# Kernel optimization log

Measured on AMD Instinct MI355X. Metric: run time of the kernel, lower is better.

Reference implementation:

```python
import jax, jax.numpy as jnp
import numpy as np

N = 100000
E = 1600000
ENC_EDGE = 32
ENC_NODE = 64
HIDDEN = 128


def setup_inputs() -> dict:
    key = jax.random.key(0)
    ks = jax.random.split(key, 8)
    x = jax.random.normal(ks[0], (N, ENC_NODE), dtype=jnp.float32)
    edge_index = jax.random.randint(ks[1], (2, E), 0, N, dtype=jnp.int64)
    edge_attr = jax.random.normal(ks[2], (E, ENC_EDGE), dtype=jnp.float32)
    u = jax.random.normal(ks[3], (256, ENC_NODE), dtype=jnp.float32)
    batch = jax.random.randint(ks[4], (N,), 0, 256, dtype=jnp.int64)
    # mlp1: Lin(ENC_EDGE+ENC_NODE -> HIDDEN), xavier_uniform weight, bias=0.01
    in1 = ENC_EDGE + ENC_NODE
    lim1 = float(np.sqrt(6.0 / (in1 + HIDDEN)))
    W1 = jax.random.uniform(ks[5], (in1, HIDDEN), minval=-lim1, maxval=lim1, dtype=jnp.float32)
    b1 = jnp.full((HIDDEN,), 0.01, dtype=jnp.float32)
    # mlp2: Lin(HIDDEN+ENC_NODE -> ENC_NODE)
    in2 = HIDDEN + ENC_NODE
    lim2 = float(np.sqrt(6.0 / (in2 + ENC_NODE)))
    W2 = jax.random.uniform(ks[6], (in2, ENC_NODE), minval=-lim2, maxval=lim2, dtype=jnp.float32)
    b2 = jnp.full((ENC_NODE,), 0.01, dtype=jnp.float32)
    return {"x": x, "edge_index": edge_index, "edge_attr": edge_attr,
            "u": u, "batch": batch, "W1": W1, "b1": b1, "W2": W2, "b2": b2}


def reference(x, edge_index, edge_attr, u, batch, W1, b1, W2, b2):
    row, col = edge_index[0], edge_index[1]
    # gather source node features, concat edge features -> [E, 96]
    msg = jnp.concatenate([x[row], edge_attr], axis=1)
    # mlp1 -> [E, HIDDEN]
    msg = msg @ W1 + b1
    # scatter_add into destination nodes -> [N, HIDDEN]
    agg = jax.ops.segment_sum(msg, col, num_segments=x.shape[0])
    # concat with node features, mlp2 -> [N, ENC_NODE]
    out = jnp.concatenate([x, agg], axis=1)
    return out @ W2 + b2
```

## Files before the change

### kernel.cpp

```cpp
#include <hip/hip_runtime.h>

#define NN 100000
#define NE 1600000
#define CAP 32
#define OVF_CAP 65536


__device__ __forceinline__ float mcat_val(const float* __restrict__ W1,
                                          const float* __restrict__ W2,
                                          int r, int j) {
    if (r < 64) return W2[r * 64 + j];
    float acc = 0.f;
    if (r < 128) {
        int i = r - 64;
        for (int h = 0; h < 128; ++h)
            acc = fmaf(W1[i * 128 + h], W2[(64 + h) * 64 + j], acc);
    } else {
        int i = r - 128;
        for (int h = 0; h < 128; ++h)
            acc = fmaf(W1[(64 + i) * 128 + h], W2[(64 + h) * 64 + j], acc);
    }
    return acc;
}

__global__ void precompute_kernel(const float* __restrict__ W1,
                                  const float* __restrict__ b1,
                                  const float* __restrict__ W2,
                                  float* __restrict__ Mcat,
                                  float* __restrict__ vb) {
    int idx = blockIdx.x * blockDim.x + threadIdx.x;
    if (idx < 160 * 64) {
        int kb = idx >> 8, j = (idx >> 2) & 63, w = idx & 3;
        Mcat[idx] = mcat_val(W1, W2, kb * 4 + w, j);
    } else if (idx < 160 * 64 + 64) {
        int j = idx - 160 * 64;
        float acc = 0.f;
        for (int h = 0; h < 128; ++h)
            acc = fmaf(b1[h], W2[(64 + h) * 64 + j], acc);
        vb[j] = acc;
    }
}

__global__ void fill_kernel(const int* __restrict__ ei,
                            int* __restrict__ cnt,
                            int* __restrict__ ovf_cnt,
                            int2* __restrict__ slots,
                            int4* __restrict__ ovf) {
    int i = blockIdx.x * blockDim.x + threadIdx.x;
    int stride = gridDim.x * blockDim.x;
    for (int e = i; e < NE; e += stride) {
        int src = ei[e];
        int dst = ei[NE + e];
        int pos = atomicAdd(&cnt[dst], 1);
        if (pos < CAP) {
            slots[dst * CAP + pos] = make_int2(src, e);
        } else {
            int op = atomicAdd(ovf_cnt, 1);
            if (op < OVF_CAP) ovf[op] = make_int4(dst, src, e, 0);
        }
    }
}

__global__ __launch_bounds__(1024, 2)
void gather_kernel(const float* __restrict__ x,
                   const float* __restrict__ ea,
                   const float* __restrict__ b2,
                   const float* __restrict__ Mcat,
                   const float* __restrict__ vb,
                   const int* __restrict__ cnt,
                   const int2* __restrict__ slots,
                   float* __restrict__ out) {
    __shared__ __align__(16) float m4[40 * 256];
    __shared__ __align__(16) float v_lds[16][160];
    __shared__ int p_lds[16][64];
    __shared__ float vb_lds[64], b2_lds[64];

    for (int i = threadIdx.x; i < 10240; i += 1024) m4[i] = Mcat[i];
    if (threadIdx.x < 64) {
        vb_lds[threadIdx.x] = vb[threadIdx.x];
        b2_lds[threadIdx.x] = b2[threadIdx.x];
    }
    __syncthreads();

    int wave = threadIdx.x >> 6;
    int lane = threadIdx.x & 63;
    int elane = lane & 31;
    int nwt = gridDim.x * 16;

    for (int n = blockIdx.x * 16 + wave; n < NN; n += nwt) {
        int dcnt = cnt[n];
        int m = dcnt < CAP ? dcnt : CAP;
        p_lds[wave][lane] = ((const int*)slots)[(size_t)n * 64 + lane];
        __threadfence_block();
        const int2* pr = (const int2*)p_lds[wave];

        float xa0 = 0.f, xa1 = 0.f, xa2 = 0.f, xa3 = 0.f;
        float e0a = 0.f, e1a = 0.f;
        int i = 0;
        for (; i + 4 <= m; i += 4) {
            int2 q0 = pr[i], q1 = pr[i + 1], q2 = pr[i + 2], q3 = pr[i + 3];
            xa0 += x[(size_t)q0.x * 64 + lane];
            xa1 += x[(size_t)q1.x * 64 + lane];
            xa2 += x[(size_t)q2.x * 64 + lane];
            xa3 += x[(size_t)q3.x * 64 + lane];
            int eA = (lane < 32) ? q0.y : q1.y;
            int eB = (lane < 32) ? q2.y : q3.y;
            e0a += ea[(size_t)eA * 32 + elane];
            e1a += ea[(size_t)eB * 32 + elane];
        }
        for (; i + 2 <= m; i += 2) {
            int2 q0 = pr[i], q1 = pr[i + 1];
            xa0 += x[(size_t)q0.x * 64 + lane];
            xa1 += x[(size_t)q1.x * 64 + lane];
            int eA = (lane < 32) ? q0.y : q1.y;
            e0a += ea[(size_t)eA * 32 + elane];
        }
        if (i < m) {
            int2 q0 = pr[i];
            xa0 += x[(size_t)q0.x * 64 + lane];
            if (lane < 32) e0a += ea[(size_t)q0.y * 32 + elane];
        }
        float xacc = (xa0 + xa1) + (xa2 + xa3);
        float eacc = e0a + e1a;
        eacc += __shfl_xor(eacc, 32);

        v_lds[wave][lane] = x[(size_t)n * 64 + lane];
        v_lds[wave][64 + lane] = xacc;
        if (lane < 32) v_lds[wave][128 + elane] = eacc;
        __threadfence_block();

        float acc = b2_lds[lane] + (float)dcnt * vb_lds[lane];
        #pragma unroll
        for (int kb = 0; kb < 40; ++kb) {
            float4 vv = *reinterpret_cast<const float4*>(&v_lds[wave][kb * 4]);
            float4 mm = *reinterpret_cast<const float4*>(&m4[kb * 256 + lane * 4]);
            acc = fmaf(vv.x, mm.x, acc);
            acc = fmaf(vv.y, mm.y, acc);
            acc = fmaf(vv.z, mm.z, acc);
            acc = fmaf(vv.w, mm.w, acc);
        }
        out[(size_t)n * 64 + lane] = acc;
    }
}

__global__ void ovf_kernel(const float* __restrict__ x,
                           const float* __restrict__ ea,
                           const float* __restrict__ Mcat,
                           const int* __restrict__ ovf_cnt,
                           const int4* __restrict__ ovf,
                           float* __restrict__ out) {
    int no = *ovf_cnt;
    if (no > OVF_CAP) no = OVF_CAP;
    int wv = (blockIdx.x * blockDim.x + threadIdx.x) >> 6;
    int lane = threadIdx.x & 63;
    int nw = (gridDim.x * blockDim.x) >> 6;
    for (int o = wv; o < no; o += nw) {
        int4 t = ovf[o];
        float acc = 0.f;
        #pragma unroll
        for (int kb = 16; kb < 32; ++kb) {
            float4 xv = *reinterpret_cast<const float4*>(&x[(size_t)t.y * 64 + (kb - 16) * 4]);
            float4 mm = *reinterpret_cast<const float4*>(&Mcat[kb * 256 + lane * 4]);
            acc = fmaf(xv.x, mm.x, acc);
            acc = fmaf(xv.y, mm.y, acc);
            acc = fmaf(xv.z, mm.z, acc);
            acc = fmaf(xv.w, mm.w, acc);
        }
        #pragma unroll
        for (int kb = 32; kb < 40; ++kb) {
            float4 av = *reinterpret_cast<const float4*>(&ea[(size_t)t.z * 32 + (kb - 32) * 4]);
            float4 mm = *reinterpret_cast<const float4*>(&Mcat[kb * 256 + lane * 4]);
            acc = fmaf(av.x, mm.x, acc);
            acc = fmaf(av.y, mm.y, acc);
            acc = fmaf(av.z, mm.z, acc);
            acc = fmaf(av.w, mm.w, acc);
        }
        atomicAdd(&out[(size_t)t.x * 64 + lane], acc);
    }
}

extern "C" void kernel_launch(void* const* d_in, const int* in_sizes, int n_in,
                              void* d_out, int out_size, void* d_ws, size_t ws_size,
                              hipStream_t stream) {
    const float* x  = (const float*)d_in[0];
    const int*   ei = (const int*)d_in[1];
    const float* ea = (const float*)d_in[2];
    const float* W1 = (const float*)d_in[5];
    const float* b1 = (const float*)d_in[6];
    const float* W2 = (const float*)d_in[7];
    const float* b2 = (const float*)d_in[8];

    float* ws      = (float*)d_ws;
    float* Mcat    = ws;
    float* vb      = ws + 10240;
    int*   cnt     = (int*)(ws + 16384);
    int*   ovf_cnt = cnt + NN;
    int2*  slots   = (int2*)(cnt + NN + 64);
    int4*  ovf     = (int4*)((int*)slots + (size_t)NN * CAP * 2);

    hipMemsetAsync(cnt, 0, (NN + 64) * sizeof(int), stream);

    precompute_kernel<<<41, 256, 0, stream>>>(W1, b1, W2, Mcat, vb);
    fill_kernel<<<2048, 256, 0, stream>>>(ei, cnt, ovf_cnt, slots, ovf);
    gather_kernel<<<512, 1024, 0, stream>>>(x, ea, b2, Mcat, vb, cnt, slots,
                                            (float*)d_out);
    ovf_kernel<<<16, 256, 0, stream>>>(x, ea, Mcat, ovf_cnt, ovf, (float*)d_out);
}
```

Baseline: 210.3 us.

## Replace per-node atomic slot fill with two-pass bucketed binning and counting sort

```diff
diff --git a/kernel.cpp b/kernel.cpp
--- a/kernel.cpp
+++ b/kernel.cpp
@@ -2,8 +2,11 @@
 
 #define NN 100000
 #define NE 1600000
-#define CAP 32
+#define NBK 196
+#define BNODES 512
+#define BCAP 8960
 #define OVF_CAP 65536
+#define EMASK 0x1FFFFF
 
 
 __device__ __forceinline__ float mcat_val(const float* __restrict__ W1,
@@ -41,23 +44,113 @@
     }
 }
 
-__global__ void fill_kernel(const int* __restrict__ ei,
-                            int* __restrict__ cnt,
-                            int* __restrict__ ovf_cnt,
-                            int2* __restrict__ slots,
-                            int4* __restrict__ ovf) {
-    int i = blockIdx.x * blockDim.x + threadIdx.x;
-    int stride = gridDim.x * blockDim.x;
-    for (int e = i; e < NE; e += stride) {
-        int src = ei[e];
-        int dst = ei[NE + e];
-        int pos = atomicAdd(&cnt[dst], 1);
-        if (pos < CAP) {
-            slots[dst * CAP + pos] = make_int2(src, e);
-        } else {
-            int op = atomicAdd(ovf_cnt, 1);
-            if (op < OVF_CAP) ovf[op] = make_int4(dst, src, e, 0);
-        }
+__device__ __forceinline__ void spill_rec(int* ovf_cnt, int4* ovf, int b, int2 r) {
+    int dst = b * BNODES + (int)((unsigned)r.y >> 21);
+    int e = r.y & EMASK;
+    int op = atomicAdd(ovf_cnt, 1);
+    if (op < OVF_CAP) ovf[op] = make_int4(dst, r.x, e, 0);
+}
+
+__global__ __launch_bounds__(1024)
+void bin_kernel(const int* __restrict__ ei,
+                int* __restrict__ gcur,
+                int* __restrict__ ovf_cnt,
+                int2* __restrict__ recs,
+                int4* __restrict__ ovf) {
+    __shared__ int2 ring[NBK][32];
+    __shared__ int cur[NBK], flushed[NBK];
+    int tid = threadIdx.x;
+    if (tid < NBK) { cur[tid] = 0; flushed[tid] = 0; }
+    __syncthreads();
+
+    const int per = NE / 256;
+    int base = blockIdx.x * per;
+    for (int it = 0; it < 7; ++it) {
+        int idx = it * 1024 + tid;
+        if (idx < per) {
+            int e = base + idx;
+            int src = ei[e], dst = ei[NE + e];
+            int b = dst >> 9;
+            int p = atomicAdd(&cur[b], 1);
+            ring[b][p & 31] = make_int2(src, ((dst & 511) << 21) | e);
+        }
+        __syncthreads();
+        if (tid < NBK) {
+            int f = flushed[tid];
+            int g8 = ((cur[tid] - f) >> 3) << 3;
+            if (g8 > 0) {
+                int gb = atomicAdd(&gcur[tid], g8);
+                int2* rb = recs + (size_t)tid * BCAP;
+                for (int k = 0; k < g8; k += 2) {
+                    int2 r0 = ring[tid][(f + k) & 31];
+                    int2 r1 = ring[tid][(f + k + 1) & 31];
+                    if (gb + k + 1 < BCAP) {
+                        *reinterpret_cast<int4*>(&rb[gb + k]) =
+                            make_int4(r0.x, r0.y, r1.x, r1.y);
+                    } else {
+                        spill_rec(ovf_cnt, ovf, tid, r0);
+                        spill_rec(ovf_cnt, ovf, tid, r1);
+                    }
+                }
+                flushed[tid] = f + g8;
+            }
+        }
+        __syncthreads();
+    }
+    if (tid < NBK) {
+        int f = flushed[tid];
+        int rem = cur[tid] - f;
+        if (rem > 0) {
+            int gb = atomicAdd(&gcur[tid], rem);
+            int2* rb = recs + (size_t)tid * BCAP;
+            for (int k = 0; k < rem; ++k) {
+                int2 r = ring[tid][(f + k) & 31];
+                if (gb + k < BCAP) rb[gb + k] = r;
+                else spill_rec(ovf_cnt, ovf, tid, r);
+            }
+        }
+    }
+}
+
+__global__ __launch_bounds__(1024)
+void sort_kernel(const int* __restrict__ gcur,
+                 const int2* __restrict__ recs,
+                 int2* __restrict__ ordered,
+                 int* __restrict__ row_start,
+                 int* __restrict__ counts) {
+    __shared__ int cnt[BNODES], s[BNODES], cur[BNODES];
+    int b = blockIdx.x, tid = threadIdx.x;
+    int nrec = gcur[b]; if (nrec > BCAP) nrec = BCAP;
+    const int2* rb = recs + (size_t)b * BCAP;
+    int2* ob = ordered + (size_t)b * BCAP;
+
+    if (tid < BNODES) cnt[tid] = 0;
+    __syncthreads();
+    for (int i = tid; i < nrec; i += 1024)
+        atomicAdd(&cnt[(unsigned)rb[i].y >> 21], 1);
+    __syncthreads();
+    if (tid < BNODES) s[tid] = cnt[tid];
+    __syncthreads();
+    for (int off = 1; off < BNODES; off <<= 1) {
+        int t = 0;
+        if (tid < BNODES && tid >= off) t = s[tid - off];
+        __syncthreads();
+        if (tid < BNODES) s[tid] += t;
+        __syncthreads();
+    }
+    int obase = b * BCAP;
+    if (tid < BNODES) {
+        int excl = s[tid] - cnt[tid];
+        cur[tid] = excl;
+        int n = b * BNODES + tid;
+        if (n < NN) { row_start[n] = obase + excl; counts[n] = cnt[tid]; }
+    }
+    __syncthreads();
+    for (int i = tid; i < nrec; i += 1024) {
+        int2 r = rb[i];
+        int dl = (unsigned)r.y >> 21;
+        int pos = atomicAdd(&cur[dl], 1);
+        ob[pos] = make_int2(r.x, r.y & EMASK);
     }
 }
 
@@ -67,12 +160,13 @@
                    const float* __restrict__ b2,
                    const float* __restrict__ Mcat,
                    const float* __restrict__ vb,
-                   const int* __restrict__ cnt,
-                   const int2* __restrict__ slots,
+                   const int* __restrict__ row_start,
+                   const int* __restrict__ counts,
+                   const int2* __restrict__ pairs,
                    float* __restrict__ out) {
     __shared__ __align__(16) float m4[40 * 256];
     __shared__ __align__(16) float v_lds[16][160];
-    __shared__ int p_lds[16][64];
+    __shared__ __align__(8)  int2  p_lds[16][64];
     __shared__ float vb_lds[64], b2_lds[64];
 
     for (int i = threadIdx.x; i < 10240; i += 1024) m4[i] = Mcat[i];
@@ -88,37 +182,42 @@
     int nwt = gridDim.x * 16;
 
     for (int n = blockIdx.x * 16 + wave; n < NN; n += nwt) {
-        int dcnt = cnt[n];
-        int m = dcnt < CAP ? dcnt : CAP;
-        p_lds[wave][lane] = ((const int*)slots)[(size_t)n * 64 + lane];
-        __threadfence_block();
-        const int2* pr = (const int2*)p_lds[wave];
-
+        int dcnt = counts[n];
+        int c = row_start[n];
         float xa0 = 0.f, xa1 = 0.f, xa2 = 0.f, xa3 = 0.f;
         float e0a = 0.f, e1a = 0.f;
-        int i = 0;
-        for (; i + 4 <= m; i += 4) {
-            int2 q0 = pr[i], q1 = pr[i + 1], q2 = pr[i + 2], q3 = pr[i + 3];
-            xa0 += x[(size_t)q0.x * 64 + lane];
-            xa1 += x[(size_t)q1.x * 64 + lane];
-            xa2 += x[(size_t)q2.x * 64 + lane];
-            xa3 += x[(size_t)q3.x * 64 + lane];
-            int eA = (lane < 32) ? q0.y : q1.y;
-            int eB = (lane < 32) ? q2.y : q3.y;
-            e0a += ea[(size_t)eA * 32 + elane];
-            e1a += ea[(size_t)eB * 32 + elane];
-        }
-        for (; i + 2 <= m; i += 2) {
-            int2 q0 = pr[i], q1 = pr[i + 1];
-            xa0 += x[(size_t)q0.x * 64 + lane];
-            xa1 += x[(size_t)q1.x * 64 + lane];
-            int eA = (lane < 32) ? q0.y : q1.y;
-            e0a += ea[(size_t)eA * 32 + elane];
-        }
-        if (i < m) {
-            int2 q0 = pr[i];
-            xa0 += x[(size_t)q0.x * 64 + lane];
-            if (lane < 32) e0a += ea[(size_t)q0.y * 32 + elane];
+        int rem = dcnt;
+        while (rem > 0) {
+            int m = rem < 64 ? rem : 64;
+            if (lane < m) p_lds[wave][lane] = pairs[c + lane];
+            __threadfence_block();
+            const int2* pr = p_lds[wave];
+            int i = 0;
+            for (; i + 4 <= m; i += 4) {
+                int2 q0 = pr[i], q1 = pr[i + 1], q2 = pr[i + 2], q3 = pr[i + 3];
+                xa0 += x[(size_t)q0.x * 64 + lane];
+                xa1 += x[(size_t)q1.x * 64 + lane];
+                xa2 += x[(size_t)q2.x * 64 + lane];
+                xa3 += x[(size_t)q3.x * 64 + lane];
+                int eA = (lane < 32) ? q0.y : q1.y;
+                int eB = (lane < 32) ? q2.y : q3.y;
+                e0a += ea[(size_t)eA * 32 + elane];
+                e1a += ea[(size_t)eB * 32 + elane];
+            }
+            for (; i + 2 <= m; i += 2) {
+                int2 q0 = pr[i], q1 = pr[i + 1];
+                xa0 += x[(size_t)q0.x * 64 + lane];
+                xa1 += x[(size_t)q1.x * 64 + lane];
+                int eA = (lane < 32) ? q0.y : q1.y;
+                e0a += ea[(size_t)eA * 32 + elane];
+            }
+            if (i < m) {
+                int2 q0 = pr[i];
+                xa0 += x[(size_t)q0.x * 64 + lane];
+                if (lane < 32) e0a += ea[(size_t)q0.y * 32 + elane];
+            }
+            rem -= m;
+            c += m;
         }
         float xacc = (xa0 + xa1) + (xa2 + xa3);
         float eacc = e0a + e1a;
@@ -146,6 +245,7 @@
 __global__ void ovf_kernel(const float* __restrict__ x,
                            const float* __restrict__ ea,
                            const float* __restrict__ Mcat,
+                           const float* __restrict__ vb,
                            const int* __restrict__ ovf_cnt,
                            const int4* __restrict__ ovf,
                            float* __restrict__ out) {
@@ -156,7 +256,7 @@
     int nw = (gridDim.x * blockDim.x) >> 6;
     for (int o = wv; o < no; o += nw) {
         int4 t = ovf[o];
-        float acc = 0.f;
+        float acc = vb[lane];
         #pragma unroll
         for (int kb = 16; kb < 32; ++kb) {
             float4 xv = *reinterpret_cast<const float4*>(&x[(size_t)t.y * 64 + (kb - 16) * 4]);
@@ -190,19 +290,23 @@
     const float* W2 = (const float*)d_in[7];
     const float* b2 = (const float*)d_in[8];
 
-    float* ws      = (float*)d_ws;
-    float* Mcat    = ws;
-    float* vb      = ws + 10240;
-    int*   cnt     = (int*)(ws + 16384);
-    int*   ovf_cnt = cnt + NN;
-    int2*  slots   = (int2*)(cnt + NN + 64);
-    int4*  ovf     = (int4*)((int*)slots + (size_t)NN * CAP * 2);
-
-    hipMemsetAsync(cnt, 0, (NN + 64) * sizeof(int), stream);
+    float* ws        = (float*)d_ws;
+    float* Mcat      = ws;
+    float* vb        = ws + 10240;
+    int*   gcur      = (int*)(ws + 10496);
+    int*   ovf_cnt   = gcur + 200;
+    int2*  recs      = (int2*)(ws + 10752);
+    int2*  ordered   = recs + (size_t)NBK * BCAP;
+    int*   row_start = (int*)(ordered + (size_t)NBK * BCAP);
+    int*   counts    = row_start + NN;
+    int4*  ovf       = (int4*)(counts + NN);
+
+    hipMemsetAsync(gcur, 0, 256 * sizeof(int), stream);
 
     precompute_kernel<<<41, 256, 0, stream>>>(W1, b1, W2, Mcat, vb);
-    fill_kernel<<<2048, 256, 0, stream>>>(ei, cnt, ovf_cnt, slots, ovf);
-    gather_kernel<<<512, 1024, 0, stream>>>(x, ea, b2, Mcat, vb, cnt, slots,
-                                            (float*)d_out);
-    ovf_kernel<<<16, 256, 0, stream>>>(x, ea, Mcat, ovf_cnt, ovf, (float*)d_out);
-}
+    bin_kernel<<<256, 1024, 0, stream>>>(ei, gcur, ovf_cnt, recs, ovf);
+    sort_kernel<<<NBK, 1024, 0, stream>>>(gcur, recs, ordered, row_start, counts);
+    gather_kernel<<<512, 1024, 0, stream>>>(x, ea, b2, Mcat, vb, row_start,
+                                            counts, ordered, (float*)d_out);
+    ovf_kernel<<<16, 256, 0, stream>>>(x, ea, Mcat, vb, ovf_cnt, ovf, (float*)d_out);
+}
```

New measurement: 180.3 us. 1.17x faster.
